# Performance work log

Hardware: AMD Instinct MI355X
Metric: run time of the kernel (lower is better)

The kernel has to match this reference:

```python
import jax, jax.numpy as jnp
import numpy as np
from jax.scipy.special import logsumexp

N, T, F, S, L = 16, 800, 90, 128, 200
NEG = -1e30
DEN_SCALE = 1.0


def setup_inputs() -> dict:
    key = jax.random.key(0)
    ks = jax.random.split(key, 6)
    # nnet_output is the output of log_softmax (per the docstring)
    logits = jax.random.normal(ks[0], (N, T, F), dtype=jnp.float32)
    nnet_output = jax.nn.log_softmax(logits, axis=-1)
    seq_idx = jnp.arange(N, dtype=jnp.int32)
    starts = jnp.zeros((N,), dtype=jnp.int32)
    nframes = jax.random.randint(ks[1], (N,), T // 2, T + 1).astype(jnp.int32)
    supervision_segments = jnp.stack([seq_idx, starts, nframes], axis=1)
    # shared denominator graph: dense log transition weights + state phone labels
    den_trans = jax.random.normal(ks[2], (S, S), dtype=jnp.float32) - 2.0
    den_labels = jax.random.randint(ks[3], (S,), 0, F).astype(jnp.int32)
    # numerator linear-chain graphs: per-utterance phone label sequences
    num_labels = jax.random.randint(ks[4], (N, L), 0, F).astype(jnp.int32)
    num_lens = jax.random.randint(ks[5], (N,), L // 2, L + 1).astype(jnp.int32)
    return {
        'nnet_output': nnet_output,
        'supervision_segments': supervision_segments,
        'den_trans': den_trans,
        'den_labels': den_labels,
        'num_labels': num_labels,
        'num_lens': num_lens,
    }


def _mmi_tot_scores(nnet_output, num_frames, den_trans, den_labels, num_labels, num_lens):
    """Log-semiring forward scores: num - den_scale * den per utterance."""
    x = jnp.transpose(nnet_output, (1, 0, 2))  # [T, N, F]
    ts = jnp.arange(T)

    # ---- denominator: shared dense WFSA, forward algorithm ----
    def den_step(alpha, inp):
        x_t, t = inp  # x_t: [N, F]
        emit = x_t[:, den_labels]  # [N, S] gather of frame log-probs
        new = logsumexp(alpha[:, :, None] + den_trans[None, :, :], axis=1) + emit
        alpha = jnp.where((t < num_frames)[:, None], new, alpha)
        return alpha, None

    a0 = jnp.full((N, S), NEG, dtype=nnet_output.dtype).at[:, 0].set(0.0)
    den_alpha, _ = jax.lax.scan(den_step, a0, (x, ts))
    den_scores = logsumexp(den_alpha, axis=1)  # [N]

    # ---- numerator: per-utterance linear chain (self-loop or advance) ----
    def num_step(alpha, inp):
        x_t, t = inp
        emit = jnp.take_along_axis(x_t, num_labels, axis=1)  # [N, L]
        body = jnp.logaddexp(alpha[:, 1:], alpha[:, :L]) + emit
        new = jnp.concatenate(
            [jnp.full((N, 1), NEG, dtype=alpha.dtype), body], axis=1)
        alpha = jnp.where((t < num_frames)[:, None], new, alpha)
        return alpha, None

    b0 = jnp.full((N, L + 1), NEG, dtype=nnet_output.dtype).at[:, 0].set(0.0)
    num_alpha, _ = jax.lax.scan(num_step, b0, (x, ts))
    num_scores = jnp.take_along_axis(num_alpha, num_lens[:, None], axis=1)[:, 0]

    return num_scores - DEN_SCALE * den_scores


def reference(nnet_output, supervision_segments, den_trans, den_labels, num_labels, num_lens):
    num_frames = supervision_segments[:, 2]
    tot = _mmi_tot_scores(nnet_output, num_frames, den_trans, den_labels,
                          num_labels, num_lens)
    # drop sequences whose score diverged (mirrors get_tot_objf_and_num_frames)
    finite = jnp.isfinite(tot) & (tot > 0.5 * NEG)
    tot_score = jnp.sum(jnp.where(finite, tot, 0.0))
    tot_frames = jnp.sum(jnp.where(finite, num_frames, 0))
    all_frames = jnp.sum(num_frames)
    return tot_score, tot_frames, all_frames
```

## Files before the change

### kernel.cpp

```cpp
#include <hip/hip_runtime.h>
#include <math.h>

#define NB 16
#define TT 800
#define FF 90
#define SS 128
#define LL 200
#define NEGV (-1e30f)

#define DNODES 16
#define DNDRX 50
#define QNODES 32
#define QDRX 25
#define BROW 26
#define NEGH (-60000.0f)
#define EPAD 228
#define LN2F 0.69314718055994531f
#define LOG2E 1.4426950408889634f

typedef __attribute__((ext_vector_type(8))) short short8;
typedef __attribute__((ext_vector_type(4))) float float4v;

static __device__ __forceinline__ unsigned short f2bf(float x) {
    union { float f; unsigned u; } v; v.f = x;
    unsigned r = (v.u + 0x7FFFu + ((v.u >> 16) & 1u)) >> 16;
    return (unsigned short)r;
}
static __device__ __forceinline__ unsigned packperm(float a, float b) {
    return __builtin_amdgcn_perm(__float_as_uint(b), __float_as_uint(a),
                                 0x07060302u);
}
static __device__ __forceinline__ int xsw(int row, int wrd) {
    return (wrd & 3) | ((((wrd >> 2) ^ (row & 7)) << 2));
}

__global__ __launch_bounds__(512, 2) void mmi_nodes(
    const float* __restrict__ x,
    const int*   __restrict__ sup,
    const float* __restrict__ trans,
    const int*   __restrict__ den_labels,
    const int*   __restrict__ num_labels,
    unsigned*    __restrict__ Pout,
    float*       __restrict__ scales8,
    _Float16*    __restrict__ Bd)
{
    __shared__ __align__(16) unsigned char SMEM[58368];
    const int tid = threadIdx.x;

    if (blockIdx.x < NB * DNODES) {
        const int bid = blockIdx.x;
        const int u  = bid >> 4;
        const int nd = bid & 15;
        const int t0 = nd * DNDRX;
        const int nf = sup[u * 3 + 2];
        unsigned* Pg = Pout + (size_t)bid * 8192;

        if (t0 >= nf) {
            #pragma unroll
            for (int k2 = 0; k2 < 16; ++k2) {
                const int ww = tid + k2 * 512;
                const int row = ww >> 6, colw = ww & 63;
                unsigned val = 0;
                if (row == 2 * colw)     val |= 0x3F80u;
                if (row == 2 * colw + 1) val |= 0x3F800000u;
                Pg[ww] = val;
            }
            if (tid < 8) scales8[bid * 8 + tid] = 0.0f;
            return;
        }

        const int w = tid >> 6, l = tid & 63;
        const int m15 = l & 15, q = l >> 4, h = m15 & 7;

        unsigned* AFs = (unsigned*)SMEM;
        #pragma unroll
        for (int i = 0; i < 16; ++i) {
            const int wi = tid + i * 512;
            const int f  = wi >> 2, j2 = wi & 3;
            const int fl = f & 63, kc = (f >> 6) & 3, mt = f >> 8;
            const int col = mt * 16 + (fl & 15);
            const int krow = kc * 32 + (fl >> 4) * 8 + 2 * j2;
            const float a = __expf(trans[(krow    ) * SS + col]);
            const float b = __expf(trans[(krow + 1) * SS + col]);
            AFs[wi] = (unsigned)f2bf(a) | ((unsigned)f2bf(b) << 16);
        }
        __syncthreads();
        short8 afrag[8][4];
        #pragma unroll
        for (int mt = 0; mt < 8; ++mt)
            #pragma unroll
            for (int kc = 0; kc < 4; ++kc)
                afrag[mt][kc] =
                    *(const short8*)(AFs + ((mt * 4 + kc) * 64 + l) * 4);
        __syncthreads();

        unsigned* Xs  = (unsigned*)SMEM;
        float* ptab   = (float*)(SMEM + 32768);

        for (int idx = tid; idx < DNDRX * SS; idx += 512) {
            const int tt = idx >> 7, d = idx & 127;
            const int fr = min(t0 + tt, TT - 1);
            ptab[idx] = __expf(x[((size_t)u * TT + fr) * FF + den_labels[d]]);
        }
        __syncthreads();

        unsigned* Xw = Xs + w * (16 * 64);
        {
            const float p0 = ptab[2 * l], p1 = ptab[2 * l + 1];
            #pragma unroll
            for (int k2 = 0; k2 < 16; ++k2) {
                const int R = w * 16 + k2;
                const float2 t2 = ((const float2*)trans)[R * 64 + l];
                Xw[k2 * 64 + xsw(k2, l)] = packperm(__expf(t2.x) * p0,
                                                    __expf(t2.y) * p1);
            }
        }

        const unsigned short* XwH = (const unsigned short*)Xw;
        const int kmax = min(DNDRX, nf - t0);
        int eacc = 0;
        float redmax = 1.0f;

        for (int k = 1; k < kmax; ++k) {
            const bool dosc = ((k & 3) == 0);
            float sc = 1.0f;
            if (dosc) {
                const float mm = fmaxf(redmax, 1e-37f);
                const int e = (int)((__float_as_uint(mm) >> 23) & 255u);
                sc = __uint_as_float((unsigned)(254 - e) << 23);
                eacc += (e - 127);
            }

            short8 bf[4];
            #pragma unroll
            for (int kc = 0; kc < 4; ++kc)
                bf[kc] = *(const short8*)(XwH + m15 * 128 +
                                          8 * (((kc << 2) | q) ^ h));

            float4v acc[8];
            #pragma unroll
            for (int mt = 0; mt < 8; ++mt) {
                float4v z = {0.f, 0.f, 0.f, 0.f};
                acc[mt] = z;
            }
            __builtin_amdgcn_s_setprio(1);
            #pragma unroll
            for (int kc = 0; kc < 4; ++kc)
                #pragma unroll
                for (int mt = 0; mt < 8; ++mt)
                    acc[mt] = __builtin_amdgcn_mfma_f32_16x16x32_bf16(
                        afrag[mt][kc], bf[kc], acc[mt], 0, 0, 0);
            __builtin_amdgcn_s_setprio(0);

            const bool dmax = ((k & 3) == 3);
            float vmax = 0.0f;
            #pragma unroll
            for (int mt = 0; mt < 8; ++mt) {
                float4 pc = *(const float4*)(ptab + k * SS + mt * 16 + 4 * q);
                if (dosc) { pc.x *= sc; pc.y *= sc; pc.z *= sc; pc.w *= sc; }
                acc[mt][0] *= pc.x;
                acc[mt][1] *= pc.y;
                acc[mt][2] *= pc.z;
                acc[mt][3] *= pc.w;
                if (dmax)
                    vmax = fmaxf(vmax,
                        fmaxf(fmaxf(acc[mt][0], acc[mt][1]),
                              fmaxf(acc[mt][2], acc[mt][3])));
            }
            if (dmax) {
                #pragma unroll
                for (int off = 32; off >= 1; off >>= 1)
                    vmax = fmaxf(vmax, __shfl_xor(vmax, off, 64));
                redmax = vmax;
            }

            #pragma unroll
            for (int mt = 0; mt < 8; ++mt) {
                uint2 pk;
                pk.x = packperm(acc[mt][0], acc[mt][1]);
                pk.y = packperm(acc[mt][2], acc[mt][3]);
                *(uint2*)(Xw + m15 * 64 +
                          4 * (((mt << 1) | (q >> 1)) ^ h) + 2 * (q & 1)) = pk;
            }
        }

        #pragma unroll
        for (int k2 = 0; k2 < 16; ++k2)
            Pg[(w * 16 + k2) * 64 + l] = Xw[k2 * 64 + xsw(k2, l)];
        if (l == 0) scales8[bid * 8 + w] = (float)eacc;
        return;
    }

    {
        float* est = (float*)(SMEM + 16);

        const int qb    = blockIdx.x - NB * DNODES;
        const int slot0 = qb * 2;
        const int u     = slot0 / QNODES;
        const int nd0   = slot0 - u * QNODES;
        const int nf    = sup[u * 3 + 2];
        const int* nlu  = num_labels + u * LL;

        for (int idx = tid; idx < 2 * QDRX * EPAD; idx += 512) {
            const int g   = idx / (QDRX * EPAD);
            const int rem = idx - g * (QDRX * EPAD);
            const int tt  = rem / EPAD;
            const int j   = rem - tt * EPAD;
            const int jj  = min(j, 199);
            const int fr  = min((nd0 + g) * QDRX + tt, TT - 1);
            est[idx] = x[((size_t)u * TT + fr) * FF + nlu[jj]] * LOG2E;
        }
        __syncthreads();

        const int g  = tid >> 8;
        const int c  = tid & 255;
        const int nd = nd0 + g;
        const int t0 = nd * QDRX;
        const int kmaxg = min(QDRX, max(nf - t0, 0));
        const float* eg = est + g * (QDRX * EPAD);

        float a[BROW];
        a[0] = 0.0f;
        #pragma unroll
        for (int d = 1; d < BROW; ++d) a[d] = NEGV;

        const float* etc = eg + (c - 1);
        for (int t = 0; t < kmaxg; ++t, etc += EPAD) {
            const int tc = t + 1;
            #pragma unroll
            for (int d = BROW - 1; d >= 1; --d) {
                if (d <= tc) {
                    const float e  = etc[d];
                    const float aa = a[d], bb = a[d - 1];
                    const float mx = fmaxf(aa, bb);
                    const float dd = fminf(aa, bb) - mx;
                    a[d] = e + mx +
                           __builtin_amdgcn_logf(
                               1.0f + __builtin_amdgcn_exp2f(dd));
                }
            }
            a[0] = (c == 0) ? NEGV : (etc[0] + a[0]);
        }

        if (c <= 200) {
            _Float16* Bg = Bd + (size_t)(slot0 + g) * 201 * BROW;
            #pragma unroll
            for (int d = 0; d < BROW; ++d) {
                const int r = c + d;
                if (r <= 200) Bg[r * BROW + d] = (_Float16)fmaxf(a[d], NEGH);
            }
            if (c < BROW - 1) {
                for (int kk = c + 1; kk < BROW; ++kk)
                    Bg[c * BROW + kk] = (_Float16)NEGH;
            }
        }
    }
}

__global__ __launch_bounds__(256) void mmi_chain(
    const unsigned short* __restrict__ Pmat,
    const _Float16* __restrict__ Bd,
    const float* __restrict__ scales8,
    const int* __restrict__ num_lens,
    const int* __restrict__ sup,
    float* __restrict__ dsc,
    int*   __restrict__ ctr,
    float* __restrict__ out)
{
    __shared__ float sh_v[SS];
    __shared__ float sh_part[8 * SS];
    __shared__ float sh_red[2];
    __shared__ float ab[2][232];
    __shared__ int sfl;

    const int tid = threadIdx.x;

    if (blockIdx.x < NB) {
        const int u = blockIdx.x;
        const int gg = tid & 31, c = tid >> 5;
        const unsigned short* Pu = Pmat + (size_t)u * DNODES * 16384;

        if (tid < SS) sh_v[tid] = (tid == 0) ? 1.0f : 0.0f;
        int   e2acc = 0;
        float sscal = 0.0f;

        uint2 curm[16], nxt[16];
        #pragma unroll
        for (int j = 0; j < 16; ++j)
            curm[j] = *(const uint2*)(Pu + (16 * c + j) * SS + 4 * gg);
        __syncthreads();

        for (int i = 0; i < DNODES; ++i) {
            if (i + 1 < DNODES) {
                const unsigned short* Pn = Pu + (size_t)(i + 1) * 16384;
                #pragma unroll
                for (int j = 0; j < 16; ++j)
                    nxt[j] = *(const uint2*)(Pn + (16 * c + j) * SS + 4 * gg);
            }
            const float* s8 = scales8 + (size_t)(u * DNODES + i) * 8;
            float gmax = s8[0];
            #pragma unroll
            for (int g2 = 1; g2 < 8; ++g2) gmax = fmaxf(gmax, s8[g2]);
            const float fgr = __builtin_amdgcn_exp2f(s8[c] - gmax);
            sscal += gmax;

            const float4* av = (const float4*)(sh_v + 16 * c);
            float4 aa[4] = {av[0], av[1], av[2], av[3]};
            const float* as = (const float*)aa;
            float4 acc = make_float4(0.f, 0.f, 0.f, 0.f);
            #pragma unroll
            for (int j = 0; j < 16; ++j) {
                const float e0 = __uint_as_float(curm[j].x << 16);
                const float e1 = __uint_as_float(curm[j].x & 0xFFFF0000u);
                const float e2 = __uint_as_float(curm[j].y << 16);
                const float e3 = __uint_as_float(curm[j].y & 0xFFFF0000u);
                acc.x = fmaf(as[j], e0, acc.x);
                acc.y = fmaf(as[j], e1, acc.y);
                acc.z = fmaf(as[j], e2, acc.z);
                acc.w = fmaf(as[j], e3, acc.w);
            }
            acc.x *= fgr; acc.y *= fgr; acc.z *= fgr; acc.w *= fgr;
            *(float4*)(sh_part + c * SS + 4 * gg) = acc;
            __syncthreads();

            float v = 0.0f;
            if (tid < SS) {
                float y = 0.0f;
                #pragma unroll
                for (int cc = 0; cc < 8; ++cc) y += sh_part[cc * SS + tid];
                v = y;
                float m = v;
                #pragma unroll
                for (int off = 32; off >= 1; off >>= 1)
                    m = fmaxf(m, __shfl_xor(m, off, 64));
                if ((tid & 63) == 0) sh_red[tid >> 6] = m;
            }
            __syncthreads();
            if (tid < SS) {
                const float mm = fmaxf(fmaxf(sh_red[0], sh_red[1]), 1e-37f);
                const int e = (int)((__float_as_uint(mm) >> 23) & 255u);
                const float inv = __uint_as_float((unsigned)(254 - e) << 23);
                e2acc += (e - 127);
                sh_v[tid] = v * inv;
            }
            #pragma unroll
            for (int j = 0; j < 16; ++j) curm[j] = nxt[j];
            __syncthreads();
        }

        if (tid < SS) {
            float s = sh_v[tid];
            #pragma unroll
            for (int off = 32; off >= 1; off >>= 1)
                s += __shfl_xor(s, off, 64);
            if ((tid & 63) == 0) sh_red[tid >> 6] = s;
        }
        __syncthreads();
        if (tid == 0)
            atomicExch(&dsc[u], LN2F * ((float)e2acc + sscal) +
                                __logf(sh_red[0] + sh_red[1]));
    } else {
        const int u = blockIdx.x - NB;
        const _Float16* Bu = Bd + (size_t)u * QNODES * 201 * BROW;
        const int r = tid;

        if (r < 232) { ab[0][r] = NEGV; ab[1][r] = NEGV; }
        float dv[BROW];
        if (r < 201) {
            #pragma unroll
            for (int k = 0; k < BROW; ++k) dv[k] = (float)Bu[r * BROW + k];
        }
        __syncthreads();
        if (r == 0) ab[0][QDRX] = 0.0f;
        __syncthreads();

        int cur = 0;
        for (int nd = 0; nd < QNODES; ++nd) {
            _Float16 nx[BROW];
            if (nd + 1 < QNODES && r < 201) {
                const _Float16* src = Bu + ((size_t)(nd + 1) * 201 + r) * BROW;
                #pragma unroll
                for (int k = 0; k < BROW; ++k) nx[k] = src[k];
            }
            float anew = NEGV;
            if (r < 201) {
                float tr[BROW];
                #pragma unroll
                for (int k = 0; k < BROW; ++k)
                    tr[k] = dv[k] + ab[cur][QDRX + r - k];
                float m = tr[0];
                #pragma unroll
                for (int k = 1; k < BROW; ++k) m = fmaxf(m, tr[k]);
                float s = 0.0f;
                #pragma unroll
                for (int k = 0; k < BROW; ++k)
                    s += __builtin_amdgcn_exp2f(tr[k] - m);
                anew = m + __builtin_amdgcn_logf(s);
            }
            if (r < 201) ab[cur ^ 1][QDRX + r] = anew;
            cur ^= 1;
            __syncthreads();
            if (r < 201) {
                #pragma unroll
                for (int k = 0; k < BROW; ++k) dv[k] = (float)nx[k];
            }
        }
        if (r == 0)
            atomicExch(&dsc[NB + u], ab[cur][QDRX + num_lens[u]] * LN2F);
    }

    __threadfence();
    if (tid == 0) sfl = (atomicAdd(ctr, 1) == 2 * NB - 1);
    __syncthreads();
    if (!sfl) return;
    __threadfence();
    if (tid < 64) {
        float tot_score = 0.0f, tot_frames = 0.0f, all_frames = 0.0f;
        if (tid < NB) {
            const float d = atomicAdd(&dsc[tid], 0.0f);
            const float n = atomicAdd(&dsc[NB + tid], 0.0f);
            const float tot = n - d;
            const int nf = sup[tid * 3 + 2];
            const bool fin = isfinite(tot) && (tot > 0.5f * NEGV);
            tot_score  = fin ? tot : 0.0f;
            tot_frames = fin ? (float)nf : 0.0f;
            all_frames = (float)nf;
        }
        #pragma unroll
        for (int off = 32; off >= 1; off >>= 1) {
            tot_score  += __shfl_xor(tot_score, off, 64);
            tot_frames += __shfl_xor(tot_frames, off, 64);
            all_frames += __shfl_xor(all_frames, off, 64);
        }
        if (tid == 0) {
            out[0] = tot_score;
            out[1] = tot_frames;
            out[2] = all_frames;
        }
    }
}

__global__ void mmi_finalize(const float* __restrict__ sc,
                             const int* __restrict__ sup,
                             float* __restrict__ out)
{
    const int tid = threadIdx.x;
    float tot_score = 0.0f, tot_frames = 0.0f, all_frames = 0.0f;
    if (tid < NB) {
        const float tot = sc[NB + tid] - sc[tid];
        const int nf = sup[tid * 3 + 2];
        const bool fin = isfinite(tot) && (tot > 0.5f * NEGV);
        tot_score  = fin ? tot : 0.0f;
        tot_frames = fin ? (float)nf : 0.0f;
        all_frames = (float)nf;
    }
    #pragma unroll
    for (int off = 32; off >= 1; off >>= 1) {
        tot_score  += __shfl_xor(tot_score, off, 64);
        tot_frames += __shfl_xor(tot_frames, off, 64);
        all_frames += __shfl_xor(all_frames, off, 64);
    }
    if (tid == 0) {
        out[0] = tot_score;
        out[1] = tot_frames;
        out[2] = all_frames;
    }
}

#define XBF (16 * FF)
__global__ __launch_bounds__(256) void mmi_forward_fb(
    const float* __restrict__ x, const int* __restrict__ sup,
    const float* __restrict__ trans, const int* __restrict__ den_labels,
    const int* __restrict__ num_labels, const int* __restrict__ num_lens,
    float* __restrict__ ws)
{
    const int tid = threadIdx.x;
    if (blockIdx.x < NB) {
        __shared__ float sh_v[SS];
        __shared__ float sh_part[8 * SS];
        __shared__ float sh_red[4];
        __shared__ __align__(16) float xbuf[2][XBF];
        const int n = blockIdx.x, nf = sup[n * 3 + 2];
        const int g = tid & 31, c = tid >> 5;
        float4 e[16];
        #pragma unroll
        for (int j = 0; j < 16; ++j) {
            const float4 t4 = *(const float4*)(trans + (size_t)(16 * c + j) * SS + 4 * g);
            e[j] = make_float4(__expf(t4.x), __expf(t4.y), __expf(t4.z), __expf(t4.w));
        }
        const int lab = (tid < SS) ? den_labels[tid & (SS - 1)] : 0;
        const float* xb = x + (size_t)n * TT * FF;
        {
            const float4* s0 = (const float4*)xb;
            float4 p0 = s0[tid]; float4 p1; if (tid < 104) p1 = s0[256 + tid];
            float4* d0 = (float4*)xbuf[0];
            d0[tid] = p0; if (tid < 104) d0[256 + tid] = p1;
        }
        if (tid < SS) sh_v[tid] = (tid == 0) ? 1.0f : 0.0f;
        float logM = 0.0f, v = 0.0f, pe = 0.0f;
        float4 pf0, pf1;
        __syncthreads();
        for (int t = 0; t < nf; ++t) {
            const int b = t >> 4;
            if (tid < SS) pe = __expf(xbuf[b & 1][(t & 15) * FF + lab]);
            float4 aa[4];
            { const float4* av = (const float4*)(sh_v + 16 * c);
              aa[0] = av[0]; aa[1] = av[1]; aa[2] = av[2]; aa[3] = av[3]; }
            const float* as = (const float*)aa;
            float4 acc = make_float4(0.f, 0.f, 0.f, 0.f);
            #pragma unroll
            for (int j = 0; j < 16; ++j) {
                acc.x = fmaf(as[j], e[j].x, acc.x); acc.y = fmaf(as[j], e[j].y, acc.y);
                acc.z = fmaf(as[j], e[j].z, acc.z); acc.w = fmaf(as[j], e[j].w, acc.w);
            }
            *(float4*)(sh_part + c * SS + 4 * g) = acc;
            if ((t & 15) == 8) {
                const int tn = (b + 1) * 16;
                if (tn < nf) {
                    const float4* s = (const float4*)(xb + (size_t)tn * FF);
                    pf0 = s[tid]; if (tid < 104) pf1 = s[256 + tid];
                }
            }
            __syncthreads();
            const bool rs = ((t & 15) == 15);
            if (tid < SS) {
                float y = 0.0f;
                #pragma unroll
                for (int cc = 0; cc < 8; ++cc) y += sh_part[cc * SS + tid];
                v = y * pe;
                if (rs) {
                    float m = v;
                    #pragma unroll
                    for (int off = 32; off >= 1; off >>= 1)
                        m = fmaxf(m, __shfl_xor(m, off, 64));
                    if ((tid & 63) == 0) sh_red[tid >> 6] = m;
                }
            }
            if (rs) {
                const int tn = (b + 1) * 16;
                if (tn < nf) {
                    float4* dst = (float4*)xbuf[(b + 1) & 1];
                    dst[tid] = pf0; if (tid < 104) dst[256 + tid] = pf1;
                }
                __syncthreads();
                if (tid < SS) {
                    float mm = fmaxf(fmaxf(sh_red[0], sh_red[1]), 1e-37f);
                    v *= (1.0f / mm); logM += __logf(mm);
                }
            }
            if (tid < SS) sh_v[tid] = v;
            __syncthreads();
        }
        if (tid < SS) {
            float ssum = v;
            #pragma unroll
            for (int off = 32; off >= 1; off >>= 1) ssum += __shfl_xor(ssum, off, 64);
            if ((tid & 63) == 0) sh_red[2 + (tid >> 6)] = ssum;
        }
        __syncthreads();
        if (tid == 0) ws[n] = logM + __logf(sh_red[2] + sh_red[3]);
    } else {
        const int w = tid >> 6, l = tid & 63;
        const int n = (blockIdx.x - NB) * 4 + w;
        const int nf = sup[n * 3 + 2];
        const float* xb = x + (size_t)n * TT * FF;
        const int* nl = num_labels + n * LL;
        int li[4];
        #pragma unroll
        for (int k = 0; k < 4; ++k) li[k] = nl[min(4 * l + k, LL - 1)];
        float a4[4] = {NEGV, NEGV, NEGV, NEGV};
        float ea[4], eb[4];
        #pragma unroll
        for (int k = 0; k < 4; ++k) ea[k] = xb[li[k]];
        { const float* xr = xb + (size_t)min(1, nf - 1) * FF;
          #pragma unroll
          for (int k = 0; k < 4; ++k) eb[k] = xr[li[k]]; }
        auto step = [&](float (&ee)[4], int t) {
            float left = __shfl_up(a4[3], 1, 64);
            if (l == 0) left = (t == 0) ? 0.0f : NEGV;
            float prev = left;
            #pragma unroll
            for (int k = 0; k < 4; ++k) {
                const float a = a4[k], b = prev;
                const float mx = fmaxf(a, b), mn = fminf(a, b);
                const float nv = mx + __logf(1.0f + __expf(mn - mx)) + ee[k];
                prev = a4[k]; a4[k] = nv;
            }
            const int t2 = min(t + 2, nf - 1);
            const float* xr = xb + (size_t)t2 * FF;
            #pragma unroll
            for (int k = 0; k < 4; ++k) ee[k] = xr[li[k]];
        };
        int t = 0;
        while (t < nf) { step(ea, t); ++t; if (t >= nf) break; step(eb, t); ++t; }
        const int idx = num_lens[n] - 1;
        if ((idx >> 2) == l) {
            const int kk = idx & 3;
            float vv = (kk == 0) ? a4[0] : (kk == 1) ? a4[1] : (kk == 2) ? a4[2] : a4[3];
            ws[NB + n] = vv;
        }
    }
}

extern "C" void kernel_launch(void* const* d_in, const int* in_sizes, int n_in,
                              void* d_out, int out_size, void* d_ws, size_t ws_size,
                              hipStream_t stream) {
    const float* x          = (const float*)d_in[0];
    const int*   sup        = (const int*)d_in[1];
    const float* trans      = (const float*)d_in[2];
    const int*   den_labels = (const int*)d_in[3];
    const int*   num_labels = (const int*)d_in[4];
    const int*   num_lens   = (const int*)d_in[5];
    float* out = (float*)d_out;

    const size_t PBYTES = (size_t)NB * DNODES * 32768;
    const size_t BBYTES = (size_t)NB * QNODES * 201 * BROW * 2;
    const size_t SCB    = (size_t)NB * DNODES * 8 * sizeof(float);
    const size_t SOFF   = PBYTES + BBYTES;
    const size_t DOFF   = SOFF + SCB;
    const size_t COFF   = DOFF + 256;
    const size_t NEEDED = COFF + 64;

    if (ws_size >= NEEDED) {
        unsigned*  Pout    = (unsigned*)d_ws;
        _Float16*  Bd      = (_Float16*)((char*)d_ws + PBYTES);
        float*     scales8 = (float*)((char*)d_ws + SOFF);
        float*     dsc     = (float*)((char*)d_ws + DOFF);
        int*       ctr     = (int*)((char*)d_ws + COFF);
        hipMemsetAsync(ctr, 0, 64, stream);
        mmi_nodes<<<dim3(512), dim3(512), 0, stream>>>(
            x, sup, trans, den_labels, num_labels, Pout, scales8, Bd);
        mmi_chain<<<dim3(2 * NB), dim3(256), 0, stream>>>(
            (const unsigned short*)d_ws, Bd, scales8, num_lens, sup,
            dsc, ctr, out);
    } else {
        float* ws = (float*)d_ws;
        mmi_forward_fb<<<dim3(20), dim3(256), 0, stream>>>(
            x, sup, trans, den_labels, num_labels, num_lens, ws);
        mmi_finalize<<<dim3(1), dim3(64), 0, stream>>>(ws, sup, out);
    }
}
```

Baseline: 184.8 us.

## Split node blocks in half, precompute MFMA A-fragments in prep kernel

```diff
diff --git a/kernel.cpp b/kernel.cpp
--- a/kernel.cpp
+++ b/kernel.cpp
@@ -10,6 +10,7 @@
 
 #define DNODES 16
 #define DNDRX 50
+#define PTROWS 25
 #define QNODES 32
 #define QDRX 25
 #define BROW 26
@@ -34,70 +35,67 @@
     return (wrd & 3) | ((((wrd >> 2) ^ (row & 7)) << 2));
 }
 
-__global__ __launch_bounds__(512, 2) void mmi_nodes(
+__global__ __launch_bounds__(256) void mmi_prep(const float* __restrict__ trans,
+                                                unsigned* __restrict__ AF) {
+    const int idx = blockIdx.x * 256 + threadIdx.x;
+    const int l  = idx & 63, fk = idx >> 6;
+    const int mt = fk >> 2, kc = fk & 3;
+    const int q  = l >> 4,  m15 = l & 15;
+    unsigned wv[4];
+    #pragma unroll
+    for (int j2 = 0; j2 < 4; ++j2) {
+        const float a = __expf(trans[(kc * 32 + q * 8 + 2 * j2    ) * SS + mt * 16 + m15]);
+        const float b = __expf(trans[(kc * 32 + q * 8 + 2 * j2 + 1) * SS + mt * 16 + m15]);
+        wv[j2] = (unsigned)f2bf(a) | ((unsigned)f2bf(b) << 16);
+    }
+    *(uint4*)(AF + 4 * idx) = make_uint4(wv[0], wv[1], wv[2], wv[3]);
+}
+
+__global__ __launch_bounds__(256, 4) void mmi_nodes(
     const float* __restrict__ x,
     const int*   __restrict__ sup,
     const float* __restrict__ trans,
     const int*   __restrict__ den_labels,
     const int*   __restrict__ num_labels,
+    const unsigned* __restrict__ AF,
     unsigned*    __restrict__ Pout,
     float*       __restrict__ scales8,
     _Float16*    __restrict__ Bd)
 {
-    __shared__ __align__(16) unsigned char SMEM[58368];
+    __shared__ __align__(16) unsigned char SMEM[29440];
     const int tid = threadIdx.x;
 
-    if (blockIdx.x < NB * DNODES) {
-        const int bid = blockIdx.x;
-        const int u  = bid >> 4;
-        const int nd = bid & 15;
+    if (blockIdx.x < 2 * NB * DNODES) {
+        const int node = blockIdx.x >> 1;
+        const int hb   = blockIdx.x & 1;
+        const int u  = node >> 4;
+        const int nd = node & 15;
         const int t0 = nd * DNDRX;
         const int nf = sup[u * 3 + 2];
-        unsigned* Pg = Pout + (size_t)bid * 8192;
+        unsigned* Pg = Pout + (size_t)node * 8192;
 
         if (t0 >= nf) {
             #pragma unroll
             for (int k2 = 0; k2 < 16; ++k2) {
-                const int ww = tid + k2 * 512;
-                const int row = ww >> 6, colw = ww & 63;
+                const int ww = tid + k2 * 256;
+                const int row = hb * 64 + (ww >> 6), colw = ww & 63;
                 unsigned val = 0;
                 if (row == 2 * colw)     val |= 0x3F80u;
                 if (row == 2 * colw + 1) val |= 0x3F800000u;
-                Pg[ww] = val;
-            }
-            if (tid < 8) scales8[bid * 8 + tid] = 0.0f;
+                Pg[row * 64 + colw] = val;
+            }
+            if (tid < 4) scales8[node * 8 + hb * 4 + tid] = 0.0f;
             return;
         }
 
         const int w = tid >> 6, l = tid & 63;
         const int m15 = l & 15, q = l >> 4, h = m15 & 7;
-
-        unsigned* AFs = (unsigned*)SMEM;
-        #pragma unroll
-        for (int i = 0; i < 16; ++i) {
-            const int wi = tid + i * 512;
-            const int f  = wi >> 2, j2 = wi & 3;
-            const int fl = f & 63, kc = (f >> 6) & 3, mt = f >> 8;
-            const int col = mt * 16 + (fl & 15);
-            const int krow = kc * 32 + (fl >> 4) * 8 + 2 * j2;
-            const float a = __expf(trans[(krow    ) * SS + col]);
-            const float b = __expf(trans[(krow + 1) * SS + col]);
-            AFs[wi] = (unsigned)f2bf(a) | ((unsigned)f2bf(b) << 16);
-        }
-        __syncthreads();
-        short8 afrag[8][4];
-        #pragma unroll
-        for (int mt = 0; mt < 8; ++mt)
-            #pragma unroll
-            for (int kc = 0; kc < 4; ++kc)
-                afrag[mt][kc] =
-                    *(const short8*)(AFs + ((mt * 4 + kc) * 64 + l) * 4);
-        __syncthreads();
+        const int R0 = hb * 64 + w * 16;
 
         unsigned* Xs  = (unsigned*)SMEM;
-        float* ptab   = (float*)(SMEM + 32768);
-
-        for (int idx = tid; idx < DNDRX * SS; idx += 512) {
+        float* ptab   = (float*)(SMEM + 16384);
+
+        for (int idx = tid; idx < PTROWS * SS; idx += 256) {
             const int tt = idx >> 7, d = idx & 127;
             const int fr = min(t0 + tt, TT - 1);
             ptab[idx] = __expf(x[((size_t)u * TT + fr) * FF + den_labels[d]]);
@@ -109,122 +107,142 @@
             const float p0 = ptab[2 * l], p1 = ptab[2 * l + 1];
             #pragma unroll
             for (int k2 = 0; k2 < 16; ++k2) {
-                const int R = w * 16 + k2;
+                const int R = R0 + k2;
                 const float2 t2 = ((const float2*)trans)[R * 64 + l];
                 Xw[k2 * 64 + xsw(k2, l)] = packperm(__expf(t2.x) * p0,
                                                     __expf(t2.y) * p1);
             }
         }
+
+        short8 afrag[8][4];
+        #pragma unroll
+        for (int mt = 0; mt < 8; ++mt)
+            #pragma unroll
+            for (int kc = 0; kc < 4; ++kc)
+                afrag[mt][kc] =
+                    *(const short8*)(AF + ((mt * 4 + kc) * 64 + l) * 4);
 
         const unsigned short* XwH = (const unsigned short*)Xw;
         const int kmax = min(DNDRX, nf - t0);
         int eacc = 0;
         float redmax = 1.0f;
 
-        for (int k = 1; k < kmax; ++k) {
-            const bool dosc = ((k & 3) == 0);
-            float sc = 1.0f;
-            if (dosc) {
-                const float mm = fmaxf(redmax, 1e-37f);
-                const int e = (int)((__float_as_uint(mm) >> 23) & 255u);
-                sc = __uint_as_float((unsigned)(254 - e) << 23);
-                eacc += (e - 127);
-            }
-
-            short8 bf[4];
-            #pragma unroll
-            for (int kc = 0; kc < 4; ++kc)
-                bf[kc] = *(const short8*)(XwH + m15 * 128 +
-                                          8 * (((kc << 2) | q) ^ h));
-
-            float4v acc[8];
-            #pragma unroll
-            for (int mt = 0; mt < 8; ++mt) {
-                float4v z = {0.f, 0.f, 0.f, 0.f};
-                acc[mt] = z;
-            }
-            __builtin_amdgcn_s_setprio(1);
-            #pragma unroll
-            for (int kc = 0; kc < 4; ++kc)
-                #pragma unroll
-                for (int mt = 0; mt < 8; ++mt)
-                    acc[mt] = __builtin_amdgcn_mfma_f32_16x16x32_bf16(
-                        afrag[mt][kc], bf[kc], acc[mt], 0, 0, 0);
-            __builtin_amdgcn_s_setprio(0);
-
-            const bool dmax = ((k & 3) == 3);
-            float vmax = 0.0f;
-            #pragma unroll
-            for (int mt = 0; mt < 8; ++mt) {
-                float4 pc = *(const float4*)(ptab + k * SS + mt * 16 + 4 * q);
-                if (dosc) { pc.x *= sc; pc.y *= sc; pc.z *= sc; pc.w *= sc; }
-                acc[mt][0] *= pc.x;
-                acc[mt][1] *= pc.y;
-                acc[mt][2] *= pc.z;
-                acc[mt][3] *= pc.w;
-                if (dmax)
-                    vmax = fmaxf(vmax,
-                        fmaxf(fmaxf(acc[mt][0], acc[mt][1]),
-                              fmaxf(acc[mt][2], acc[mt][3])));
-            }
-            if (dmax) {
-                #pragma unroll
-                for (int off = 32; off >= 1; off >>= 1)
-                    vmax = fmaxf(vmax, __shfl_xor(vmax, off, 64));
-                redmax = vmax;
-            }
-
-            #pragma unroll
-            for (int mt = 0; mt < 8; ++mt) {
-                uint2 pk;
-                pk.x = packperm(acc[mt][0], acc[mt][1]);
-                pk.y = packperm(acc[mt][2], acc[mt][3]);
-                *(uint2*)(Xw + m15 * 64 +
-                          4 * (((mt << 1) | (q >> 1)) ^ h) + 2 * (q & 1)) = pk;
-            }
+        int kbeg = 1;
+        for (int ph = 0; ph < 2 && kbeg < kmax; ++ph) {
+            const int kend = min(kmax, PTROWS * (ph + 1));
+            const int kofs = ph * PTROWS;
+            if (ph == 1) {
+                __syncthreads();
+                for (int idx = tid; idx < PTROWS * SS; idx += 256) {
+                    const int tt = PTROWS + (idx >> 7), d = idx & 127;
+                    const int fr = min(t0 + tt, TT - 1);
+                    ptab[idx] = __expf(x[((size_t)u * TT + fr) * FF +
+                                         den_labels[d]]);
+                }
+                __syncthreads();
+            }
+
+            for (int k = kbeg; k < kend; ++k) {
+                const bool dosc = ((k & 3) == 0);
+                float sc = 1.0f;
+                if (dosc) {
+                    const float mm = fmaxf(redmax, 1e-37f);
+                    const int e = (int)((__float_as_uint(mm) >> 23) & 255u);
+                    sc = __uint_as_float((unsigned)(254 - e) << 23);
+                    eacc += (e - 127);
+                }
+
+                short8 bf[4];
+                #pragma unroll
+                for (int kc = 0; kc < 4; ++kc)
+                    bf[kc] = *(const short8*)(XwH + m15 * 128 +
+                                              8 * (((kc << 2) | q) ^ h));
+
+                float4v acc[8];
+                #pragma unroll
+                for (int mt = 0; mt < 8; ++mt) {
+                    float4v z = {0.f, 0.f, 0.f, 0.f};
+                    acc[mt] = z;
+                }
+                __builtin_amdgcn_s_setprio(1);
+                #pragma unroll
+                for (int kc = 0; kc < 4; ++kc)
+                    #pragma unroll
+                    for (int mt = 0; mt < 8; ++mt)
+                        acc[mt] = __builtin_amdgcn_mfma_f32_16x16x32_bf16(
+                            afrag[mt][kc], bf[kc], acc[mt], 0, 0, 0);
+                __builtin_amdgcn_s_setprio(0);
+
+                const bool dmax = ((k & 3) == 3);
+                float vmax = 0.0f;
+                #pragma unroll
+                for (int mt = 0; mt < 8; ++mt) {
+                    float4 pc = *(const float4*)(ptab + (k - kofs) * SS +
+                                                 mt * 16 + 4 * q);
+                    if (dosc) { pc.x *= sc; pc.y *= sc; pc.z *= sc; pc.w *= sc; }
+                    acc[mt][0] *= pc.x;
+                    acc[mt][1] *= pc.y;
+                    acc[mt][2] *= pc.z;
+                    acc[mt][3] *= pc.w;
+                    if (dmax)
+                        vmax = fmaxf(vmax,
+                            fmaxf(fmaxf(acc[mt][0], acc[mt][1]),
+                                  fmaxf(acc[mt][2], acc[mt][3])));
+                }
+                if (dmax) {
+                    #pragma unroll
+                    for (int off = 32; off >= 1; off >>= 1)
+                        vmax = fmaxf(vmax, __shfl_xor(vmax, off, 64));
+                    redmax = vmax;
+                }
+
+                #pragma unroll
+                for (int mt = 0; mt < 8; ++mt) {
+                    uint2 pk;
+                    pk.x = packperm(acc[mt][0], acc[mt][1]);
+                    pk.y = packperm(acc[mt][2], acc[mt][3]);
+                    *(uint2*)(Xw + m15 * 64 +
+                              4 * (((mt << 1) | (q >> 1)) ^ h) + 2 * (q & 1)) = pk;
+                }
+            }
+            kbeg = kend;
         }
 
         #pragma unroll
         for (int k2 = 0; k2 < 16; ++k2)
-            Pg[(w * 16 + k2) * 64 + l] = Xw[k2 * 64 + xsw(k2, l)];
-        if (l == 0) scales8[bid * 8 + w] = (float)eacc;
+            Pg[(R0 + k2) * 64 + l] = Xw[k2 * 64 + xsw(k2, l)];
+        if (l == 0) scales8[node * 8 + hb * 4 + w] = (float)eacc;
         return;
     }
 
     {
-        float* est = (float*)(SMEM + 16);
-
-        const int qb    = blockIdx.x - NB * DNODES;
-        const int slot0 = qb * 2;
-        const int u     = slot0 / QNODES;
-        const int nd0   = slot0 - u * QNODES;
-        const int nf    = sup[u * 3 + 2];
-        const int* nlu  = num_labels + u * LL;
-
-        for (int idx = tid; idx < 2 * QDRX * EPAD; idx += 512) {
-            const int g   = idx / (QDRX * EPAD);
-            const int rem = idx - g * (QDRX * EPAD);
-            const int tt  = rem / EPAD;
-            const int j   = rem - tt * EPAD;
+        float* est = (float*)SMEM;
+
+        const int slot = blockIdx.x - 2 * NB * DNODES;
+        const int u    = slot >> 5;
+        const int nd   = slot & 31;
+        const int nf   = sup[u * 3 + 2];
+        const int* nlu = num_labels + u * LL;
+
+        for (int idx = tid; idx < QDRX * EPAD; idx += 256) {
+            const int tt  = idx / EPAD;
+            const int j   = idx - tt * EPAD;
             const int jj  = min(j, 199);
-            const int fr  = min((nd0 + g) * QDRX + tt, TT - 1);
+            const int fr  = min(nd * QDRX + tt, TT - 1);
             est[idx] = x[((size_t)u * TT + fr) * FF + nlu[jj]] * LOG2E;
         }
         __syncthreads();
 
-        const int g  = tid >> 8;
-        const int c  = tid & 255;
-        const int nd = nd0 + g;
+        const int c  = tid;
         const int t0 = nd * QDRX;
         const int kmaxg = min(QDRX, max(nf - t0, 0));
-        const float* eg = est + g * (QDRX * EPAD);
 
         float a[BROW];
         a[0] = 0.0f;
         #pragma unroll
         for (int d = 1; d < BROW; ++d) a[d] = NEGV;
 
-        const float* etc = eg + (c - 1);
+        const float* etc = est + (c - 1);
         for (int t = 0; t < kmaxg; ++t, etc += EPAD) {
             const int tc = t + 1;
             #pragma unroll
@@ -243,7 +261,7 @@
         }
 
         if (c <= 200) {
-            _Float16* Bg = Bd + (size_t)(slot0 + g) * 201 * BROW;
+            _Float16* Bg = Bd + (size_t)slot * 201 * BROW;
             #pragma unroll
             for (int d = 0; d < BROW; ++d) {
                 const int r = c + d;
@@ -619,7 +637,8 @@
     const size_t SOFF   = PBYTES + BBYTES;
     const size_t DOFF   = SOFF + SCB;
     const size_t COFF   = DOFF + 256;
-    const size_t NEEDED = COFF + 64;
+    const size_t AOFF   = COFF + 256;
+    const size_t NEEDED = AOFF + 2048 * 16;
 
     if (ws_size >= NEEDED) {
         unsigned*  Pout    = (unsigned*)d_ws;
@@ -627,9 +646,11 @@
         float*     scales8 = (float*)((char*)d_ws + SOFF);
         float*     dsc     = (float*)((char*)d_ws + DOFF);
         int*       ctr     = (int*)((char*)d_ws + COFF);
+        unsigned*  AF      = (unsigned*)((char*)d_ws + AOFF);
         hipMemsetAsync(ctr, 0, 64, stream);
-        mmi_nodes<<<dim3(512), dim3(512), 0, stream>>>(
-            x, sup, trans, den_labels, num_labels, Pout, scales8, Bd);
+        mmi_prep<<<dim3(8), dim3(256), 0, stream>>>(trans, AF);
+        mmi_nodes<<<dim3(1024), dim3(256), 0, stream>>>(
+            x, sup, trans, den_labels, num_labels, AF, Pout, scales8, Bd);
         mmi_chain<<<dim3(2 * NB), dim3(256), 0, stream>>>(
             (const unsigned short*)d_ws, Bd, scales8, num_lens, sup,
             dsc, ctr, out);
```

Result: slower. 347.7 us (+88.2%).

## Double-depth prefetch and wider blocks in chain kernel with padded fp16 rows

Applied to the files above, without the earlier changes.

```diff
diff --git a/kernel.cpp b/kernel.cpp
--- a/kernel.cpp
+++ b/kernel.cpp
@@ -13,6 +13,7 @@
 #define QNODES 32
 #define QDRX 25
 #define BROW 26
+#define BST 28
 #define NEGH (-60000.0f)
 #define EPAD 228
 #define LN2F 0.69314718055994531f
@@ -20,6 +21,7 @@
 
 typedef __attribute__((ext_vector_type(8))) short short8;
 typedef __attribute__((ext_vector_type(4))) float float4v;
+typedef _Float16 h4 __attribute__((ext_vector_type(4)));
 
 static __device__ __forceinline__ unsigned short f2bf(float x) {
     union { float f; unsigned u; } v; v.f = x;
@@ -243,21 +245,21 @@
         }
 
         if (c <= 200) {
-            _Float16* Bg = Bd + (size_t)(slot0 + g) * 201 * BROW;
+            _Float16* Bg = Bd + (size_t)(slot0 + g) * 201 * BST;
             #pragma unroll
             for (int d = 0; d < BROW; ++d) {
                 const int r = c + d;
-                if (r <= 200) Bg[r * BROW + d] = (_Float16)fmaxf(a[d], NEGH);
+                if (r <= 200) Bg[r * BST + d] = (_Float16)fmaxf(a[d], NEGH);
             }
             if (c < BROW - 1) {
                 for (int kk = c + 1; kk < BROW; ++kk)
-                    Bg[c * BROW + kk] = (_Float16)NEGH;
-            }
-        }
-    }
-}
-
-__global__ __launch_bounds__(256) void mmi_chain(
+                    Bg[c * BST + kk] = (_Float16)NEGH;
+            }
+        }
+    }
+}
+
+__global__ __launch_bounds__(512) void mmi_chain(
     const unsigned short* __restrict__ Pmat,
     const _Float16* __restrict__ Bd,
     const float* __restrict__ scales8,
@@ -268,7 +270,7 @@
     float* __restrict__ out)
 {
     __shared__ float sh_v[SS];
-    __shared__ float sh_part[8 * SS];
+    __shared__ float sh_part[16 * SS];
     __shared__ float sh_red[2];
     __shared__ float ab[2][232];
     __shared__ int sfl;
@@ -284,36 +286,39 @@
         int   e2acc = 0;
         float sscal = 0.0f;
 
-        uint2 curm[16], nxt[16];
-        #pragma unroll
-        for (int j = 0; j < 16; ++j)
-            curm[j] = *(const uint2*)(Pu + (16 * c + j) * SS + 4 * gg);
+        uint2 cur[8], nx1[8], nx2[8];
+        #pragma unroll
+        for (int j = 0; j < 8; ++j)
+            cur[j] = *(const uint2*)(Pu + (8 * c + j) * SS + 4 * gg);
+        #pragma unroll
+        for (int j = 0; j < 8; ++j)
+            nx1[j] = *(const uint2*)(Pu + 16384 + (8 * c + j) * SS + 4 * gg);
         __syncthreads();
 
         for (int i = 0; i < DNODES; ++i) {
-            if (i + 1 < DNODES) {
-                const unsigned short* Pn = Pu + (size_t)(i + 1) * 16384;
-                #pragma unroll
-                for (int j = 0; j < 16; ++j)
-                    nxt[j] = *(const uint2*)(Pn + (16 * c + j) * SS + 4 * gg);
+            if (i + 2 < DNODES) {
+                const unsigned short* Pn = Pu + (size_t)(i + 2) * 16384;
+                #pragma unroll
+                for (int j = 0; j < 8; ++j)
+                    nx2[j] = *(const uint2*)(Pn + (8 * c + j) * SS + 4 * gg);
             }
             const float* s8 = scales8 + (size_t)(u * DNODES + i) * 8;
             float gmax = s8[0];
             #pragma unroll
             for (int g2 = 1; g2 < 8; ++g2) gmax = fmaxf(gmax, s8[g2]);
-            const float fgr = __builtin_amdgcn_exp2f(s8[c] - gmax);
+            const float fgr = __builtin_amdgcn_exp2f(s8[c >> 1] - gmax);
             sscal += gmax;
 
-            const float4* av = (const float4*)(sh_v + 16 * c);
-            float4 aa[4] = {av[0], av[1], av[2], av[3]};
+            const float4* av = (const float4*)(sh_v + 8 * c);
+            float4 aa[2] = {av[0], av[1]};
             const float* as = (const float*)aa;
             float4 acc = make_float4(0.f, 0.f, 0.f, 0.f);
             #pragma unroll
-            for (int j = 0; j < 16; ++j) {
-                const float e0 = __uint_as_float(curm[j].x << 16);
-                const float e1 = __uint_as_float(curm[j].x & 0xFFFF0000u);
-                const float e2 = __uint_as_float(curm[j].y << 16);
-                const float e3 = __uint_as_float(curm[j].y & 0xFFFF0000u);
+            for (int j = 0; j < 8; ++j) {
+                const float e0 = __uint_as_float(cur[j].x << 16);
+                const float e1 = __uint_as_float(cur[j].x & 0xFFFF0000u);
+                const float e2 = __uint_as_float(cur[j].y << 16);
+                const float e3 = __uint_as_float(cur[j].y & 0xFFFF0000u);
                 acc.x = fmaf(as[j], e0, acc.x);
                 acc.y = fmaf(as[j], e1, acc.y);
                 acc.z = fmaf(as[j], e2, acc.z);
@@ -327,7 +332,7 @@
             if (tid < SS) {
                 float y = 0.0f;
                 #pragma unroll
-                for (int cc = 0; cc < 8; ++cc) y += sh_part[cc * SS + tid];
+                for (int cc = 0; cc < 16; ++cc) y += sh_part[cc * SS + tid];
                 v = y;
                 float m = v;
                 #pragma unroll
@@ -344,7 +349,7 @@
                 sh_v[tid] = v * inv;
             }
             #pragma unroll
-            for (int j = 0; j < 16; ++j) curm[j] = nxt[j];
+            for (int j = 0; j < 8; ++j) { cur[j] = nx1[j]; nx1[j] = nx2[j]; }
             __syncthreads();
         }
 
@@ -361,14 +366,22 @@
                                 __logf(sh_red[0] + sh_red[1]));
     } else {
         const int u = blockIdx.x - NB;
-        const _Float16* Bu = Bd + (size_t)u * QNODES * 201 * BROW;
+        const _Float16* Bu = Bd + (size_t)u * QNODES * 201 * BST;
         const int r = tid;
+        const bool act = (r < 201);
 
         if (r < 232) { ab[0][r] = NEGV; ab[1][r] = NEGV; }
+        h4 nx1[7], nx2[7];
         float dv[BROW];
-        if (r < 201) {
-            #pragma unroll
-            for (int k = 0; k < BROW; ++k) dv[k] = (float)Bu[r * BROW + k];
+        if (act) {
+            const h4* s0 = (const h4*)(Bu + (size_t)r * BST);
+            #pragma unroll
+            for (int t7 = 0; t7 < 7; ++t7) nx1[t7] = s0[t7];
+            #pragma unroll
+            for (int k = 0; k < BROW; ++k) dv[k] = (float)nx1[k >> 2][k & 3];
+            const h4* s1 = (const h4*)(Bu + ((size_t)201 + r) * BST);
+            #pragma unroll
+            for (int t7 = 0; t7 < 7; ++t7) nx1[t7] = s1[t7];
         }
         __syncthreads();
         if (r == 0) ab[0][QDRX] = 0.0f;
@@ -376,14 +389,13 @@
 
         int cur = 0;
         for (int nd = 0; nd < QNODES; ++nd) {
-            _Float16 nx[BROW];
-            if (nd + 1 < QNODES && r < 201) {
-                const _Float16* src = Bu + ((size_t)(nd + 1) * 201 + r) * BROW;
-                #pragma unroll
-                for (int k = 0; k < BROW; ++k) nx[k] = src[k];
+            if (nd + 2 < QNODES && act) {
+                const h4* src = (const h4*)(Bu + ((size_t)(nd + 2) * 201 + r) * BST);
+                #pragma unroll
+                for (int t7 = 0; t7 < 7; ++t7) nx2[t7] = src[t7];
             }
             float anew = NEGV;
-            if (r < 201) {
+            if (act) {
                 float tr[BROW];
                 #pragma unroll
                 for (int k = 0; k < BROW; ++k)
@@ -397,12 +409,14 @@
                     s += __builtin_amdgcn_exp2f(tr[k] - m);
                 anew = m + __builtin_amdgcn_logf(s);
             }
-            if (r < 201) ab[cur ^ 1][QDRX + r] = anew;
+            if (act) ab[cur ^ 1][QDRX + r] = anew;
             cur ^= 1;
             __syncthreads();
-            if (r < 201) {
-                #pragma unroll
-                for (int k = 0; k < BROW; ++k) dv[k] = (float)nx[k];
+            if (act) {
+                #pragma unroll
+                for (int k = 0; k < BROW; ++k) dv[k] = (float)nx1[k >> 2][k & 3];
+                #pragma unroll
+                for (int t7 = 0; t7 < 7; ++t7) nx1[t7] = nx2[t7];
             }
         }
         if (r == 0)
@@ -614,12 +628,12 @@
     float* out = (float*)d_out;
 
     const size_t PBYTES = (size_t)NB * DNODES * 32768;
-    const size_t BBYTES = (size_t)NB * QNODES * 201 * BROW * 2;
+    const size_t BBYTES = (size_t)NB * QNODES * 201 * BST * 2;
     const size_t SCB    = (size_t)NB * DNODES * 8 * sizeof(float);
     const size_t SOFF   = PBYTES + BBYTES;
     const size_t DOFF   = SOFF + SCB;
     const size_t COFF   = DOFF + 256;
-    const size_t NEEDED = COFF + 64;
+    const size_t NEEDED = COFF + 256;
 
     if (ws_size >= NEEDED) {
         unsigned*  Pout    = (unsigned*)d_ws;
@@ -630,7 +644,7 @@
         hipMemsetAsync(ctr, 0, 64, stream);
         mmi_nodes<<<dim3(512), dim3(512), 0, stream>>>(
             x, sup, trans, den_labels, num_labels, Pout, scales8, Bd);
-        mmi_chain<<<dim3(2 * NB), dim3(256), 0, stream>>>(
+        mmi_chain<<<dim3(2 * NB), dim3(512), 0, stream>>>(
             (const unsigned short*)d_ws, Bd, scales8, num_lens, sup,
             dsc, ctr, out);
     } else {
```

Result: slower. 197.2 us (+6.7%).
